# Kernel optimization log

Hardware: AMD Instinct MI355X
Metric: run time of the kernel (lower is better)

The kernel has to match this reference:

```python
import jax, jax.numpy as jnp
import numpy as np

N = 20000   # nodes
E = 320000  # edges
H = 4       # attention heads
GAT_SLOPE = 0.2   # DGL GATv2Conv internal leaky_relu slope
ACT_SLOPE = 0.01  # nn.LeakyReLU default slope


def gatv2_layer(h, src, dst, Wl, Wr, attn, b):
    """DGL GATv2Conv (share_weights=False, bias=True, eval mode).
    h: [N, Fin]; Wl/Wr: [Fin, H*D]; attn: [H, D]; b: [H*D]. Returns [N, H, D]."""
    n = h.shape[0]
    Hh, D = attn.shape
    fs = (h @ Wl).reshape(n, Hh, D)  # source projection
    fd = (h @ Wr).reshape(n, Hh, D)  # destination projection
    # edge-wise GATv2 score: a^T leaky_relu(Wl h_u + Wr h_v)
    e = jax.nn.leaky_relu(fs[src] + fd[dst], negative_slope=GAT_SLOPE)  # [E,H,D]
    logit = jnp.einsum('ehd,hd->eh', e, attn)  # [E,H]
    # edge softmax over incoming edges of each dst node (numerically stable)
    m = jax.ops.segment_max(logit, dst, num_segments=n)
    a = jnp.exp(logit - m[dst])
    s = jax.ops.segment_sum(a, dst, num_segments=n)
    alpha = a / s[dst]  # [E,H]
    out = jax.ops.segment_sum(alpha[:, :, None] * fs[src], dst, num_segments=n)
    return out + b.reshape(1, Hh, D)


def setup_inputs() -> dict:
    key = jax.random.key(0)
    ks = jax.random.split(key, 16)

    def w(k, shape, fan_in):
        return (jax.random.normal(k, shape, jnp.float32) / np.float32(np.sqrt(fan_in)))

    return {
        'n_feat': jax.random.normal(ks[0], (N, 512), jnp.float32),
        'src': jax.random.randint(ks[1], (E,), 0, N, jnp.int32),
        'dst': jax.random.randint(ks[2], (E,), 0, N, jnp.int32),
        # layer 0: 512 -> H x 128
        'Wl0': w(ks[3], (512, H * 128), 512), 'Wr0': w(ks[4], (512, H * 128), 512),
        'attn0': w(ks[5], (H, 128), 128), 'b0': jnp.zeros((H * 128,), jnp.float32),
        # layer 1: 128 -> H x 128
        'Wl1': w(ks[6], (128, H * 128), 128), 'Wr1': w(ks[7], (128, H * 128), 128),
        'attn1': w(ks[8], (H, 128), 128), 'b1': jnp.zeros((H * 128,), jnp.float32),
        # layer 2 (output): 128 -> H x 64
        'Wl2': w(ks[9], (128, H * 64), 128), 'Wr2': w(ks[10], (128, H * 64), 128),
        'attn2': w(ks[11], (H, 64), 64), 'b2': jnp.zeros((H * 64,), jnp.float32),
    }


def reference(n_feat, src, dst, Wl0, Wr0, attn0, b0, Wl1, Wr1, attn1, b1,
              Wl2, Wr2, attn2, b2):
    h = n_feat.reshape(n_feat.shape[0], -1)  # nn.Flatten
    for (Wl, Wr, attn, b) in ((Wl0, Wr0, attn0, b0),
                              (Wl1, Wr1, attn1, b1),
                              (Wl2, Wr2, attn2, b2)):
        h = gatv2_layer(h, src, dst, Wl, Wr, attn, b)  # [N,H,D]
        h = h.mean(axis=1)                              # head mean
        h = jax.nn.leaky_relu(h, negative_slope=ACT_SLOPE)
    # dgl.mean_nodes: per-graph mean readout (single graph -> [1, out])
    return h.mean(axis=0, keepdims=True)
```

## Files before the change

### kernel.cpp

```cpp
#include <hip/hip_runtime.h>
#include <hip/hip_bf16.h>
#include <stdint.h>


#define GAT_SLOPE 0.2f
#define ACT_SLOPE 0.01f
#define MAXDEG 64

typedef _Float16 half8 __attribute__((ext_vector_type(8)));
typedef _Float16 v2h __attribute__((ext_vector_type(2)));
typedef float floatx4 __attribute__((ext_vector_type(4)));

struct TransDesc {
  const float* src;
  _Float16* dst;
  int K, M, off;
};
struct PreArgs {
  TransDesc d[6];
  int wTotal;
  const float* nf;
  _Float16* A0;
  int aTotal;
  const int* src;
  const int* dst;
  int* counts;
  int* pcsrc;
  int E;
};

__global__ __launch_bounds__(256) void preproc_kernel(PreArgs pa) {
  int i = blockIdx.x * 256 + threadIdx.x;
  const int total = pa.wTotal + pa.aTotal + pa.E;
  if (i >= total) return;
  if (i < pa.wTotal) {
    int q = 0;
#pragma unroll
    for (int j = 1; j < 6; ++j)
      if (i >= pa.d[j].off) q = j;
    int local = i - pa.d[q].off;
    int K = pa.d[q].K, M = pa.d[q].M;
    int m = local / K, k = local % K;
    pa.d[q].dst[local] = (_Float16)pa.d[q].src[(size_t)k * M + m];
  } else if (i < pa.wTotal + pa.aTotal) {
    int j = i - pa.wTotal;
    pa.A0[j] = (_Float16)pa.nf[j];
  } else {
    int e = i - pa.wTotal - pa.aTotal;
    int d = pa.dst[e];
    int pos = atomicAdd(&pa.counts[d], 1);
    if (pos < MAXDEG) pa.pcsrc[(size_t)d * MAXDEG + pos] = pa.src[e];
  }
}

__device__ __forceinline__ void gload_lds16(const _Float16* g, _Float16* l) {
  __builtin_amdgcn_global_load_lds(
      (__attribute__((address_space(1))) unsigned int*)g,
      (__attribute__((address_space(3))) unsigned int*)l, 16, 0, 0);
}

#define TM 128
#define TN 128
#define TK 32

__global__ __launch_bounds__(256) void gemm_mfma_dual_kernel(
    const _Float16* __restrict__ A, const _Float16* __restrict__ B0,
    const _Float16* __restrict__ B1, _Float16* __restrict__ C0,
    _Float16* __restrict__ C1, int Nrow, int K, int M, int nStrips,
    int nbxLog2) {
  const int id = blockIdx.x;
  const int xcd = id & 7;
  const int s = id >> 3;
  const int nbx = 1 << nbxLog2;
  const int col = s & (nbx - 1);
  const int chunk = s >> nbxLog2;
  const int strip = chunk * 8 + xcd;
  if (strip >= nStrips) return;

  const int nb = nbx >> 1;
  const bool second = col >= nb;
  const _Float16* B = second ? B1 : B0;
  _Float16* C = second ? C1 : C0;
  const int bn = (second ? col - nb : col) * TN;
  const int bm = strip * TM;

  __shared__ __align__(16) _Float16 As[TM * TK];
  __shared__ __align__(16) _Float16 Bs[TN * TK];

  const int tid = threadIdx.x;
  const int w = tid >> 6;
  const int lane = tid & 63;
  const int wr = w >> 1;
  const int wc = w & 1;
  const int quad = lane >> 4;
  const int lr = lane & 15;

  const int lrow = lane >> 2;
  const int loff = (lane & 3) * 8;

  floatx4 acc[4][4];
#pragma unroll
  for (int i = 0; i < 4; ++i)
#pragma unroll
    for (int j = 0; j < 4; ++j) acc[i][j] = (floatx4){0.f, 0.f, 0.f, 0.f};

  const int KT = K / TK;
  for (int kt = 0; kt < KT; ++kt) {
    const int k0 = kt * TK;
#pragma unroll
    for (int half = 0; half < 2; ++half) {
      const int r0 = w * 32 + half * 16;
      int ga = bm + r0 + lrow;
      if (ga >= Nrow) ga = Nrow - 1;
      gload_lds16(A + (size_t)ga * K + k0 + loff, As + r0 * TK);
      gload_lds16(B + (size_t)(bn + r0 + lrow) * K + k0 + loff, Bs + r0 * TK);
    }
    __syncthreads();

    half8 ar[4], br[4];
#pragma unroll
    for (int i = 0; i < 4; ++i) {
      int row = wr * 64 + i * 16 + lr;
      ar[i] = *(const half8*)(As + row * TK + quad * 8);
    }
#pragma unroll
    for (int j = 0; j < 4; ++j) {
      int colr = wc * 64 + j * 16 + lr;
      br[j] = *(const half8*)(Bs + colr * TK + quad * 8);
    }
#pragma unroll
    for (int i = 0; i < 4; ++i)
#pragma unroll
      for (int j = 0; j < 4; ++j)
        acc[i][j] = __builtin_amdgcn_mfma_f32_16x16x32_f16(ar[i], br[j],
                                                           acc[i][j], 0, 0, 0);
    __syncthreads();
  }

#pragma unroll
  for (int i = 0; i < 4; ++i) {
#pragma unroll
    for (int r = 0; r < 4; ++r) {
      int row = bm + wr * 64 + i * 16 + quad * 4 + r;
      if (row >= Nrow) continue;
#pragma unroll
      for (int j = 0; j < 4; ++j) {
        int colc = bn + wc * 64 + j * 16 + lr;
        C[(size_t)row * M + colc] = (_Float16)acc[i][j][r];
      }
    }
  }
}

template <int D>
__global__ __launch_bounds__(128) void node_attn_kernel(
    const _Float16* __restrict__ fs, const _Float16* __restrict__ fd,
    const int* __restrict__ counts, const int* __restrict__ pcsrc,
    const float* __restrict__ attn, const float* __restrict__ bias,
    float* __restrict__ hout, _Float16* __restrict__ oh, int N) {
  constexpr int HD = 4 * D;
  constexpr int R = HD / 64;
  constexpr int R2 = R / 2;
  typedef _Float16 halfR __attribute__((ext_vector_type(R)));
  union Frag {
    halfR v;
    v2h h[R2];
    _Float16 s[R];
  };
  const int v = blockIdx.x;
  if (v >= N) return;
  const int wid = threadIdx.x >> 6;
  const int lane = threadIdx.x & 63;

  const v2h slope2 = {(_Float16)GAT_SLOPE, (_Float16)GAT_SLOPE};

  Frag fdv;
  fdv.v = *(const halfR*)(fd + (size_t)v * HD + lane * R);
  v2h ar2[R2];
#pragma unroll
  for (int j = 0; j < R2; ++j) {
    ar2[j][0] = (_Float16)attn[lane * R + 2 * j];
    ar2[j][1] = (_Float16)attn[lane * R + 2 * j + 1];
  }

  float m = -INFINITY, l = 0.f;
  float O[R];
#pragma unroll
  for (int i = 0; i < R; ++i) O[i] = 0.f;

  const int cnt = min(counts[v], MAXDEG);
  const int* elist = pcsrc + (size_t)v * MAXDEG;
  const int mid = (cnt + 1) >> 1;
  int k = wid ? mid : 0;
  const int ke = wid ? cnt : mid;

  for (; k + 3 < ke; k += 4) {
    const int s0 = elist[k];
    const int s1 = elist[k + 1];
    const int s2 = elist[k + 2];
    const int s3 = elist[k + 3];
    Frag t0, t1, t2, t3;
    t0.v = *(const halfR*)(fs + (size_t)s0 * HD + lane * R);
    t1.v = *(const halfR*)(fs + (size_t)s1 * HD + lane * R);
    t2.v = *(const halfR*)(fs + (size_t)s2 * HD + lane * R);
    t3.v = *(const halfR*)(fs + (size_t)s3 * HD + lane * R);
    float p0 = 0.f, p1 = 0.f, p2 = 0.f, p3 = 0.f;
#pragma unroll
    for (int j = 0; j < R2; ++j) {
      v2h x0 = t0.h[j] + fdv.h[j];
      v2h x1 = t1.h[j] + fdv.h[j];
      v2h x2 = t2.h[j] + fdv.h[j];
      v2h x3 = t3.h[j] + fdv.h[j];
      x0 = __builtin_elementwise_max(x0, x0 * slope2);
      x1 = __builtin_elementwise_max(x1, x1 * slope2);
      x2 = __builtin_elementwise_max(x2, x2 * slope2);
      x3 = __builtin_elementwise_max(x3, x3 * slope2);
      p0 = __builtin_amdgcn_fdot2(ar2[j], x0, p0, false);
      p1 = __builtin_amdgcn_fdot2(ar2[j], x1, p1, false);
      p2 = __builtin_amdgcn_fdot2(ar2[j], x2, p2, false);
      p3 = __builtin_amdgcn_fdot2(ar2[j], x3, p3, false);
    }
#pragma unroll
    for (int off = 1; off <= 8; off <<= 1) {
      p0 += __shfl_xor(p0, off, 64);
      p1 += __shfl_xor(p1, off, 64);
      p2 += __shfl_xor(p2, off, 64);
      p3 += __shfl_xor(p3, off, 64);
    }
    const float mq = fmaxf(fmaxf(p0, p1), fmaxf(p2, p3));
    const float w0 = __expf(p0 - mq);
    const float w1 = __expf(p1 - mq);
    const float w2 = __expf(p2 - mq);
    const float w3 = __expf(p3 - mq);
    const float mnew = fmaxf(m, mq);
    const float sc = __expf(m - mnew);
    const float sq = __expf(mq - mnew);
    l = l * sc + (w0 + w1 + w2 + w3) * sq;
#pragma unroll
    for (int i = 0; i < R; ++i) {
      float acc = (float)t0.s[i] * w0;
      acc = fmaf((float)t1.s[i], w1, acc);
      acc = fmaf((float)t2.s[i], w2, acc);
      acc = fmaf((float)t3.s[i], w3, acc);
      O[i] = fmaf(O[i], sc, sq * acc);
    }
    m = mnew;
  }
  for (; k < ke; ++k) {
    const int s0 = elist[k];
    Frag t0;
    t0.v = *(const halfR*)(fs + (size_t)s0 * HD + lane * R);
    float p0 = 0.f;
#pragma unroll
    for (int j = 0; j < R2; ++j) {
      v2h x0 = t0.h[j] + fdv.h[j];
      x0 = __builtin_elementwise_max(x0, x0 * slope2);
      p0 = __builtin_amdgcn_fdot2(ar2[j], x0, p0, false);
    }
#pragma unroll
    for (int off = 1; off <= 8; off <<= 1) p0 += __shfl_xor(p0, off, 64);
    const float mnew = fmaxf(m, p0);
    const float sc = __expf(m - mnew);
    const float p = __expf(p0 - mnew);
    l = l * sc + p;
#pragma unroll
    for (int i = 0; i < R; ++i) O[i] = fmaf(O[i], sc, p * (float)t0.s[i]);
    m = mnew;
  }

  __shared__ float sO[64 * R];
  __shared__ float sM[64];
  __shared__ float sL[64];
  if (wid == 1) {
    sM[lane] = m;
    sL[lane] = l;
#pragma unroll
    for (int i = 0; i < R; ++i) sO[lane * R + i] = O[i];
  }
  __syncthreads();
  if (wid == 1) return;
  {
    const float m1 = sM[lane];
    const float l1 = sL[lane];
    const float mstar = fmaxf(m, m1);
    const float a0 = (l > 0.f) ? __expf(m - mstar) : 0.f;
    const float a1 = (l1 > 0.f) ? __expf(m1 - mstar) : 0.f;
    l = l * a0 + l1 * a1;
#pragma unroll
    for (int i = 0; i < R; ++i) O[i] = O[i] * a0 + sO[lane * R + i] * a1;
  }

  const float inv = (l > 0.f) ? 1.f / l : 0.f;
#pragma unroll
  for (int i = 0; i < R; ++i) O[i] = O[i] * inv + bias[lane * R + i];
#pragma unroll
  for (int i = 0; i < R; ++i) {
    O[i] += __shfl_xor(O[i], 16, 64);
    O[i] += __shfl_xor(O[i], 32, 64);
    float x = O[i] * 0.25f;
    O[i] = x > 0.f ? x : x * ACT_SLOPE;
  }
  if (lane < 16) {
    const size_t base = (size_t)v * D + lane * R;
    if (hout) {
#pragma unroll
      for (int i = 0; i < R; ++i) hout[base + i] = O[i];
    }
    if (oh) {
#pragma unroll
      for (int i = 0; i < R; ++i) oh[base + i] = (_Float16)O[i];
    }
  }
}

__global__ __launch_bounds__(64) void final_mean_kernel(
    const float* __restrict__ h, float* __restrict__ out, int N) {
  const int d = threadIdx.x;
  float acc = 0.f;
  for (int n = blockIdx.x; n < N; n += gridDim.x) acc += h[(size_t)n * 64 + d];
  atomicAdd(&out[d], acc / (float)N);
}

extern "C" void kernel_launch(void* const* d_in, const int* in_sizes, int n_in,
                              void* d_out, int out_size, void* d_ws,
                              size_t ws_size, hipStream_t stream) {
  const float* n_feat = (const float*)d_in[0];
  const int* src = (const int*)d_in[1];
  const int* dst = (const int*)d_in[2];
  const float* Wl[3] = {(const float*)d_in[3], (const float*)d_in[7],
                        (const float*)d_in[11]};
  const float* Wr[3] = {(const float*)d_in[4], (const float*)d_in[8],
                        (const float*)d_in[12]};
  const float* attn[3] = {(const float*)d_in[5], (const float*)d_in[9],
                          (const float*)d_in[13]};
  const float* bias[3] = {(const float*)d_in[6], (const float*)d_in[10],
                          (const float*)d_in[14]};

  const int N = in_sizes[0] / 512;
  const int E = in_sizes[1];
  const int Kdim[3] = {512, 128, 128};
  const int Mdim[3] = {512, 512, 256};

  char* ws = (char*)d_ws;
  size_t o = 0;
  auto alloc = [&](size_t bytes) {
    void* p = ws + o;
    o += (bytes + 15) & ~(size_t)15;
    return p;
  };
  _Float16* fs = (_Float16*)alloc((size_t)N * 512 * 2);
  _Float16* fd = (_Float16*)alloc((size_t)N * 512 * 2);
  _Float16* A0 = (_Float16*)alloc((size_t)N * 512 * 2);
  _Float16* h1 = (_Float16*)alloc((size_t)N * 128 * 2);
  _Float16* h2 = (_Float16*)alloc((size_t)N * 128 * 2);
  float* hfin = (float*)alloc((size_t)N * 64 * 4);
  _Float16 *WlT[3], *WrT[3];
  for (int L = 0; L < 3; ++L) {
    size_t sz = (size_t)Kdim[L] * Mdim[L] * 2;
    WlT[L] = (_Float16*)alloc(sz);
    WrT[L] = (_Float16*)alloc(sz);
  }
  int* counts = (int*)alloc((size_t)N * 4);
  int* pcsrc = (int*)alloc((size_t)N * MAXDEG * 4);

  hipMemsetAsync(counts, 0, (size_t)N * sizeof(int), stream);
  {
    PreArgs pa;
    int off = 0;
    for (int L = 0; L < 3; ++L) {
      pa.d[2 * L] = {Wl[L], WlT[L], Kdim[L], Mdim[L], off};
      off += Kdim[L] * Mdim[L];
      pa.d[2 * L + 1] = {Wr[L], WrT[L], Kdim[L], Mdim[L], off};
      off += Kdim[L] * Mdim[L];
    }
    pa.wTotal = off;
    pa.nf = n_feat;
    pa.A0 = A0;
    pa.aTotal = N * 512;
    pa.src = src;
    pa.dst = dst;
    pa.counts = counts;
    pa.pcsrc = pcsrc;
    pa.E = E;
    int total = pa.wTotal + pa.aTotal + pa.E;
    preproc_kernel<<<(total + 255) / 256, 256, 0, stream>>>(pa);
  }

  const _Float16* Ain[3] = {A0, h1, h2};

  const int nStrips = (N + TM - 1) / TM;
  const int S8 = ((nStrips + 7) / 8) * 8;

  for (int L = 0; L < 3; ++L) {
    const int K = Kdim[L], M = Mdim[L];
    const int nbx = 2 * M / TN;
    const int nbxLog2 = (nbx == 8) ? 3 : 2;
    gemm_mfma_dual_kernel<<<S8 * nbx, 256, 0, stream>>>(
        Ain[L], WlT[L], WrT[L], fs, fd, N, K, M, nStrips, nbxLog2);
    if (L == 0) {
      node_attn_kernel<128><<<N, 128, 0, stream>>>(fs, fd, counts, pcsrc,
                                                   attn[L], bias[L], nullptr,
                                                   h1, N);
    } else if (L == 1) {
      node_attn_kernel<128><<<N, 128, 0, stream>>>(fs, fd, counts, pcsrc,
                                                   attn[L], bias[L], nullptr,
                                                   h2, N);
    } else {
      node_attn_kernel<64><<<N, 128, 0, stream>>>(fs, fd, counts, pcsrc,
                                                  attn[L], bias[L], hfin,
                                                  nullptr, N);
    }
  }

  hipMemsetAsync(d_out, 0, 64 * sizeof(float), stream);
  final_mean_kernel<<<256, 64, 0, stream>>>(hfin, (float*)d_out, N);
}
```

Measured before the change: 357.6 us.

## Use one wave per node in attention, fuse final mean, drop output memset

The node attention kernel now gives each 64-lane wave a whole node instead of splitting a node's edges across two waves and merging them through shared memory. Blocks hold four waves, so four nodes run per block. The last layer reduces its outputs into a shared-memory accumulator and atomically adds the mean straight into the output. This removes the hfin buffer, the final mean kernel and the output memset, whose zeroing moves into the preprocessing kernel. The cost is that per-node latency is no longer split across waves, and the last layer uses shared-memory atomics plus a grid-stride loop over 1024 blocks.

```diff
diff --git a/kernel.cpp b/kernel.cpp
--- a/kernel.cpp
+++ b/kernel.cpp
@@ -6,18 +6,18 @@
 #define GAT_SLOPE 0.2f
 #define ACT_SLOPE 0.01f
 #define MAXDEG 64
+#define TM 128
+#define TN 128
+#define TK 32
 
 typedef _Float16 half8 __attribute__((ext_vector_type(8)));
 typedef _Float16 v2h __attribute__((ext_vector_type(2)));
 typedef float floatx4 __attribute__((ext_vector_type(4)));
 
-struct TransDesc {
-  const float* src;
-  _Float16* dst;
-  int K, M, off;
-};
 struct PreArgs {
-  TransDesc d[6];
+  const float* W[6];
+  _Float16* WT[6];
+  int wK[6], wM[6], wOff[6];
   int wTotal;
   const float* nf;
   _Float16* A0;
@@ -27,26 +27,29 @@
   int* counts;
   int* pcsrc;
   int E;
+  float* dout;
 };
 
 __global__ __launch_bounds__(256) void preproc_kernel(PreArgs pa) {
   int i = blockIdx.x * 256 + threadIdx.x;
-  const int total = pa.wTotal + pa.aTotal + pa.E;
+  const int total = pa.wTotal + pa.aTotal + 64 + pa.E;
   if (i >= total) return;
   if (i < pa.wTotal) {
     int q = 0;
 #pragma unroll
     for (int j = 1; j < 6; ++j)
-      if (i >= pa.d[j].off) q = j;
-    int local = i - pa.d[q].off;
-    int K = pa.d[q].K, M = pa.d[q].M;
+      if (i >= pa.wOff[j]) q = j;
+    int local = i - pa.wOff[q];
+    int K = pa.wK[q], M = pa.wM[q];
     int m = local / K, k = local % K;
-    pa.d[q].dst[local] = (_Float16)pa.d[q].src[(size_t)k * M + m];
+    pa.WT[q][local] = (_Float16)pa.W[q][(size_t)k * M + m];
   } else if (i < pa.wTotal + pa.aTotal) {
     int j = i - pa.wTotal;
     pa.A0[j] = (_Float16)pa.nf[j];
+  } else if (i < pa.wTotal + pa.aTotal + 64) {
+    pa.dout[i - pa.wTotal - pa.aTotal] = 0.f;
   } else {
-    int e = i - pa.wTotal - pa.aTotal;
+    int e = i - pa.wTotal - pa.aTotal - 64;
     int d = pa.dst[e];
     int pos = atomicAdd(&pa.counts[d], 1);
     if (pos < MAXDEG) pa.pcsrc[(size_t)d * MAXDEG + pos] = pa.src[e];
@@ -58,10 +61,6 @@
       (__attribute__((address_space(1))) unsigned int*)g,
       (__attribute__((address_space(3))) unsigned int*)l, 16, 0, 0);
 }
-
-#define TM 128
-#define TN 128
-#define TK 32
 
 __global__ __launch_bounds__(256) void gemm_mfma_dual_kernel(
     const _Float16* __restrict__ A, const _Float16* __restrict__ B0,
@@ -94,7 +93,6 @@
   const int wc = w & 1;
   const int quad = lane >> 4;
   const int lr = lane & 15;
-
   const int lrow = lane >> 2;
   const int loff = (lane & 3) * 8;
 
@@ -152,12 +150,12 @@
   }
 }
 
-template <int D>
-__global__ __launch_bounds__(128) void node_attn_kernel(
+template <int D, bool LAST>
+__global__ __launch_bounds__(256) void node_attn_kernel(
     const _Float16* __restrict__ fs, const _Float16* __restrict__ fd,
     const int* __restrict__ counts, const int* __restrict__ pcsrc,
-    const float* __restrict__ attn, const float* __restrict__ bias,
-    float* __restrict__ hout, _Float16* __restrict__ oh, int N) {
+    const float* __restrict__ aw, const float* __restrict__ bias,
+    _Float16* __restrict__ oh, float* __restrict__ dout, int N) {
   constexpr int HD = 4 * D;
   constexpr int R = HD / 64;
   constexpr int R2 = R / 2;
@@ -167,158 +165,141 @@
     v2h h[R2];
     _Float16 s[R];
   };
-  const int v = blockIdx.x;
-  if (v >= N) return;
+  __shared__ float facc[64];
   const int wid = threadIdx.x >> 6;
   const int lane = threadIdx.x & 63;
-
   const v2h slope2 = {(_Float16)GAT_SLOPE, (_Float16)GAT_SLOPE};
 
-  Frag fdv;
-  fdv.v = *(const halfR*)(fd + (size_t)v * HD + lane * R);
+  if (LAST) {
+    if (threadIdx.x < 64) facc[threadIdx.x] = 0.f;
+    __syncthreads();
+  }
+
   v2h ar2[R2];
 #pragma unroll
   for (int j = 0; j < R2; ++j) {
-    ar2[j][0] = (_Float16)attn[lane * R + 2 * j];
-    ar2[j][1] = (_Float16)attn[lane * R + 2 * j + 1];
-  }
-
-  float m = -INFINITY, l = 0.f;
-  float O[R];
-#pragma unroll
-  for (int i = 0; i < R; ++i) O[i] = 0.f;
-
-  const int cnt = min(counts[v], MAXDEG);
-  const int* elist = pcsrc + (size_t)v * MAXDEG;
-  const int mid = (cnt + 1) >> 1;
-  int k = wid ? mid : 0;
-  const int ke = wid ? cnt : mid;
-
-  for (; k + 3 < ke; k += 4) {
-    const int s0 = elist[k];
-    const int s1 = elist[k + 1];
-    const int s2 = elist[k + 2];
-    const int s3 = elist[k + 3];
-    Frag t0, t1, t2, t3;
-    t0.v = *(const halfR*)(fs + (size_t)s0 * HD + lane * R);
-    t1.v = *(const halfR*)(fs + (size_t)s1 * HD + lane * R);
-    t2.v = *(const halfR*)(fs + (size_t)s2 * HD + lane * R);
-    t3.v = *(const halfR*)(fs + (size_t)s3 * HD + lane * R);
-    float p0 = 0.f, p1 = 0.f, p2 = 0.f, p3 = 0.f;
-#pragma unroll
-    for (int j = 0; j < R2; ++j) {
-      v2h x0 = t0.h[j] + fdv.h[j];
-      v2h x1 = t1.h[j] + fdv.h[j];
-      v2h x2 = t2.h[j] + fdv.h[j];
-      v2h x3 = t3.h[j] + fdv.h[j];
-      x0 = __builtin_elementwise_max(x0, x0 * slope2);
-      x1 = __builtin_elementwise_max(x1, x1 * slope2);
-      x2 = __builtin_elementwise_max(x2, x2 * slope2);
-      x3 = __builtin_elementwise_max(x3, x3 * slope2);
-      p0 = __builtin_amdgcn_fdot2(ar2[j], x0, p0, false);
-      p1 = __builtin_amdgcn_fdot2(ar2[j], x1, p1, false);
-      p2 = __builtin_amdgcn_fdot2(ar2[j], x2, p2, false);
-      p3 = __builtin_amdgcn_fdot2(ar2[j], x3, p3, false);
-    }
-#pragma unroll
-    for (int off = 1; off <= 8; off <<= 1) {
-      p0 += __shfl_xor(p0, off, 64);
-      p1 += __shfl_xor(p1, off, 64);
-      p2 += __shfl_xor(p2, off, 64);
-      p3 += __shfl_xor(p3, off, 64);
-    }
-    const float mq = fmaxf(fmaxf(p0, p1), fmaxf(p2, p3));
-    const float w0 = __expf(p0 - mq);
-    const float w1 = __expf(p1 - mq);
-    const float w2 = __expf(p2 - mq);
-    const float w3 = __expf(p3 - mq);
-    const float mnew = fmaxf(m, mq);
-    const float sc = __expf(m - mnew);
-    const float sq = __expf(mq - mnew);
-    l = l * sc + (w0 + w1 + w2 + w3) * sq;
-#pragma unroll
-    for (int i = 0; i < R; ++i) {
-      float acc = (float)t0.s[i] * w0;
-      acc = fmaf((float)t1.s[i], w1, acc);
-      acc = fmaf((float)t2.s[i], w2, acc);
-      acc = fmaf((float)t3.s[i], w3, acc);
-      O[i] = fmaf(O[i], sc, sq * acc);
-    }
-    m = mnew;
-  }
-  for (; k < ke; ++k) {
-    const int s0 = elist[k];
-    Frag t0;
-    t0.v = *(const halfR*)(fs + (size_t)s0 * HD + lane * R);
-    float p0 = 0.f;
-#pragma unroll
-    for (int j = 0; j < R2; ++j) {
-      v2h x0 = t0.h[j] + fdv.h[j];
-      x0 = __builtin_elementwise_max(x0, x0 * slope2);
-      p0 = __builtin_amdgcn_fdot2(ar2[j], x0, p0, false);
-    }
-#pragma unroll
-    for (int off = 1; off <= 8; off <<= 1) p0 += __shfl_xor(p0, off, 64);
-    const float mnew = fmaxf(m, p0);
-    const float sc = __expf(m - mnew);
-    const float p = __expf(p0 - mnew);
-    l = l * sc + p;
-#pragma unroll
-    for (int i = 0; i < R; ++i) O[i] = fmaf(O[i], sc, p * (float)t0.s[i]);
-    m = mnew;
-  }
-
-  __shared__ float sO[64 * R];
-  __shared__ float sM[64];
-  __shared__ float sL[64];
-  if (wid == 1) {
-    sM[lane] = m;
-    sL[lane] = l;
-#pragma unroll
-    for (int i = 0; i < R; ++i) sO[lane * R + i] = O[i];
-  }
-  __syncthreads();
-  if (wid == 1) return;
-  {
-    const float m1 = sM[lane];
-    const float l1 = sL[lane];
-    const float mstar = fmaxf(m, m1);
-    const float a0 = (l > 0.f) ? __expf(m - mstar) : 0.f;
-    const float a1 = (l1 > 0.f) ? __expf(m1 - mstar) : 0.f;
-    l = l * a0 + l1 * a1;
-#pragma unroll
-    for (int i = 0; i < R; ++i) O[i] = O[i] * a0 + sO[lane * R + i] * a1;
-  }
-
-  const float inv = (l > 0.f) ? 1.f / l : 0.f;
-#pragma unroll
-  for (int i = 0; i < R; ++i) O[i] = O[i] * inv + bias[lane * R + i];
-#pragma unroll
-  for (int i = 0; i < R; ++i) {
-    O[i] += __shfl_xor(O[i], 16, 64);
-    O[i] += __shfl_xor(O[i], 32, 64);
-    float x = O[i] * 0.25f;
-    O[i] = x > 0.f ? x : x * ACT_SLOPE;
-  }
-  if (lane < 16) {
-    const size_t base = (size_t)v * D + lane * R;
-    if (hout) {
-#pragma unroll
-      for (int i = 0; i < R; ++i) hout[base + i] = O[i];
-    }
-    if (oh) {
-#pragma unroll
-      for (int i = 0; i < R; ++i) oh[base + i] = (_Float16)O[i];
-    }
-  }
-}
-
-__global__ __launch_bounds__(64) void final_mean_kernel(
-    const float* __restrict__ h, float* __restrict__ out, int N) {
-  const int d = threadIdx.x;
-  float acc = 0.f;
-  for (int n = blockIdx.x; n < N; n += gridDim.x) acc += h[(size_t)n * 64 + d];
-  atomicAdd(&out[d], acc / (float)N);
+    ar2[j][0] = (_Float16)aw[lane * R + 2 * j];
+    ar2[j][1] = (_Float16)aw[lane * R + 2 * j + 1];
+  }
+  float br[R];
+#pragma unroll
+  for (int i = 0; i < R; ++i) br[i] = bias[lane * R + i];
+
+  for (int v0 = blockIdx.x * 4; v0 < N; v0 += gridDim.x * 4) {
+    const int v = v0 + wid;
+    if (v < N) {
+      Frag fdv;
+      fdv.v = *(const halfR*)(fd + (size_t)v * HD + lane * R);
+      float m = -INFINITY, l = 0.f;
+      float O[R];
+#pragma unroll
+      for (int i = 0; i < R; ++i) O[i] = 0.f;
+
+      const int cnt = min(counts[v], MAXDEG);
+      const int* elist = pcsrc + (size_t)v * MAXDEG;
+      int k = 0;
+      for (; k + 3 < cnt; k += 4) {
+        const int s0 = elist[k];
+        const int s1 = elist[k + 1];
+        const int s2 = elist[k + 2];
+        const int s3 = elist[k + 3];
+        Frag t0, t1, t2, t3;
+        t0.v = *(const halfR*)(fs + (size_t)s0 * HD + lane * R);
+        t1.v = *(const halfR*)(fs + (size_t)s1 * HD + lane * R);
+        t2.v = *(const halfR*)(fs + (size_t)s2 * HD + lane * R);
+        t3.v = *(const halfR*)(fs + (size_t)s3 * HD + lane * R);
+        float p0 = 0.f, p1 = 0.f, p2 = 0.f, p3 = 0.f;
+#pragma unroll
+        for (int j = 0; j < R2; ++j) {
+          v2h x0 = t0.h[j] + fdv.h[j];
+          v2h x1 = t1.h[j] + fdv.h[j];
+          v2h x2 = t2.h[j] + fdv.h[j];
+          v2h x3 = t3.h[j] + fdv.h[j];
+          x0 = __builtin_elementwise_max(x0, x0 * slope2);
+          x1 = __builtin_elementwise_max(x1, x1 * slope2);
+          x2 = __builtin_elementwise_max(x2, x2 * slope2);
+          x3 = __builtin_elementwise_max(x3, x3 * slope2);
+          p0 = __builtin_amdgcn_fdot2(ar2[j], x0, p0, false);
+          p1 = __builtin_amdgcn_fdot2(ar2[j], x1, p1, false);
+          p2 = __builtin_amdgcn_fdot2(ar2[j], x2, p2, false);
+          p3 = __builtin_amdgcn_fdot2(ar2[j], x3, p3, false);
+        }
+#pragma unroll
+        for (int off = 1; off <= 8; off <<= 1) {
+          p0 += __shfl_xor(p0, off, 64);
+          p1 += __shfl_xor(p1, off, 64);
+          p2 += __shfl_xor(p2, off, 64);
+          p3 += __shfl_xor(p3, off, 64);
+        }
+        const float mq = fmaxf(fmaxf(p0, p1), fmaxf(p2, p3));
+        const float w0 = __expf(p0 - mq);
+        const float w1 = __expf(p1 - mq);
+        const float w2 = __expf(p2 - mq);
+        const float w3 = __expf(p3 - mq);
+        const float mnew = fmaxf(m, mq);
+        const float sc = __expf(m - mnew);
+        const float sq = __expf(mq - mnew);
+        l = l * sc + (w0 + w1 + w2 + w3) * sq;
+#pragma unroll
+        for (int i = 0; i < R; ++i) {
+          float acc = (float)t0.s[i] * w0;
+          acc = fmaf((float)t1.s[i], w1, acc);
+          acc = fmaf((float)t2.s[i], w2, acc);
+          acc = fmaf((float)t3.s[i], w3, acc);
+          O[i] = fmaf(O[i], sc, sq * acc);
+        }
+        m = mnew;
+      }
+      for (; k < cnt; ++k) {
+        const int s0 = elist[k];
+        Frag t0;
+        t0.v = *(const halfR*)(fs + (size_t)s0 * HD + lane * R);
+        float p0 = 0.f;
+#pragma unroll
+        for (int j = 0; j < R2; ++j) {
+          v2h x0 = t0.h[j] + fdv.h[j];
+          x0 = __builtin_elementwise_max(x0, x0 * slope2);
+          p0 = __builtin_amdgcn_fdot2(ar2[j], x0, p0, false);
+        }
+#pragma unroll
+        for (int off = 1; off <= 8; off <<= 1) p0 += __shfl_xor(p0, off, 64);
+        const float mnew = fmaxf(m, p0);
+        const float sc = __expf(m - mnew);
+        const float p = __expf(p0 - mnew);
+        l = l * sc + p;
+#pragma unroll
+        for (int i = 0; i < R; ++i) O[i] = fmaf(O[i], sc, p * (float)t0.s[i]);
+        m = mnew;
+      }
+
+      const float inv = (l > 0.f) ? 1.f / l : 0.f;
+#pragma unroll
+      for (int i = 0; i < R; ++i) O[i] = O[i] * inv + br[i];
+#pragma unroll
+      for (int i = 0; i < R; ++i) {
+        O[i] += __shfl_xor(O[i], 16, 64);
+        O[i] += __shfl_xor(O[i], 32, 64);
+        float x = O[i] * 0.25f;
+        O[i] = x > 0.f ? x : x * ACT_SLOPE;
+      }
+      if (lane < 16) {
+        if (!LAST) {
+          const size_t base = (size_t)v * D + lane * R;
+#pragma unroll
+          for (int i = 0; i < R; ++i) oh[base + i] = (_Float16)O[i];
+        } else {
+#pragma unroll
+          for (int i = 0; i < R; ++i) atomicAdd(&facc[lane * R + i], O[i]);
+        }
+      }
+    }
+  }
+
+  if (LAST) {
+    __syncthreads();
+    if (threadIdx.x < 64)
+      atomicAdd(&dout[threadIdx.x], facc[threadIdx.x] / (float)N);
+  }
 }
 
 extern "C" void kernel_launch(void* const* d_in, const int* in_sizes, int n_in,
@@ -331,8 +312,8 @@
                         (const float*)d_in[11]};
   const float* Wr[3] = {(const float*)d_in[4], (const float*)d_in[8],
                         (const float*)d_in[12]};
-  const float* attn[3] = {(const float*)d_in[5], (const float*)d_in[9],
-                          (const float*)d_in[13]};
+  const float* attnw[3] = {(const float*)d_in[5], (const float*)d_in[9],
+                           (const float*)d_in[13]};
   const float* bias[3] = {(const float*)d_in[6], (const float*)d_in[10],
                           (const float*)d_in[14]};
 
@@ -353,24 +334,30 @@
   _Float16* A0 = (_Float16*)alloc((size_t)N * 512 * 2);
   _Float16* h1 = (_Float16*)alloc((size_t)N * 128 * 2);
   _Float16* h2 = (_Float16*)alloc((size_t)N * 128 * 2);
-  float* hfin = (float*)alloc((size_t)N * 64 * 4);
-  _Float16 *WlT[3], *WrT[3];
+  _Float16* WT[6];
   for (int L = 0; L < 3; ++L) {
     size_t sz = (size_t)Kdim[L] * Mdim[L] * 2;
-    WlT[L] = (_Float16*)alloc(sz);
-    WrT[L] = (_Float16*)alloc(sz);
+    WT[2 * L] = (_Float16*)alloc(sz);
+    WT[2 * L + 1] = (_Float16*)alloc(sz);
   }
   int* counts = (int*)alloc((size_t)N * 4);
   int* pcsrc = (int*)alloc((size_t)N * MAXDEG * 4);
 
   hipMemsetAsync(counts, 0, (size_t)N * sizeof(int), stream);
+
   {
     PreArgs pa;
     int off = 0;
     for (int L = 0; L < 3; ++L) {
-      pa.d[2 * L] = {Wl[L], WlT[L], Kdim[L], Mdim[L], off};
+      pa.W[2 * L] = Wl[L];
+      pa.W[2 * L + 1] = Wr[L];
+      pa.WT[2 * L] = WT[2 * L];
+      pa.WT[2 * L + 1] = WT[2 * L + 1];
+      pa.wK[2 * L] = pa.wK[2 * L + 1] = Kdim[L];
+      pa.wM[2 * L] = pa.wM[2 * L + 1] = Mdim[L];
+      pa.wOff[2 * L] = off;
       off += Kdim[L] * Mdim[L];
-      pa.d[2 * L + 1] = {Wr[L], WrT[L], Kdim[L], Mdim[L], off};
+      pa.wOff[2 * L + 1] = off;
       off += Kdim[L] * Mdim[L];
     }
     pa.wTotal = off;
@@ -382,11 +369,14 @@
     pa.counts = counts;
     pa.pcsrc = pcsrc;
     pa.E = E;
-    int total = pa.wTotal + pa.aTotal + pa.E;
+    pa.dout = (float*)d_out;
+    int total = pa.wTotal + pa.aTotal + 64 + E;
     preproc_kernel<<<(total + 255) / 256, 256, 0, stream>>>(pa);
   }
 
   const _Float16* Ain[3] = {A0, h1, h2};
+  _Float16* WlT[3] = {WT[0], WT[2], WT[4]};
+  _Float16* WrT[3] = {WT[1], WT[3], WT[5]};
 
   const int nStrips = (N + TM - 1) / TM;
   const int S8 = ((nStrips + 7) / 8) * 8;
@@ -398,20 +388,14 @@
     gemm_mfma_dual_kernel<<<S8 * nbx, 256, 0, stream>>>(
         Ain[L], WlT[L], WrT[L], fs, fd, N, K, M, nStrips, nbxLog2);
     if (L == 0) {
-      node_attn_kernel<128><<<N, 128, 0, stream>>>(fs, fd, counts, pcsrc,
-                                                   attn[L], bias[L], nullptr,
-                                                   h1, N);
+      node_attn_kernel<128, false><<<(N + 3) / 4, 256, 0, stream>>>(
+          fs, fd, counts, pcsrc, attnw[0], bias[0], h1, nullptr, N);
     } else if (L == 1) {
-      node_attn_kernel<128><<<N, 128, 0, stream>>>(fs, fd, counts, pcsrc,
-                                                   attn[L], bias[L], nullptr,
-                                                   h2, N);
+      node_attn_kernel<128, false><<<(N + 3) / 4, 256, 0, stream>>>(
+          fs, fd, counts, pcsrc, attnw[1], bias[1], h2, nullptr, N);
     } else {
-      node_attn_kernel<64><<<N, 128, 0, stream>>>(fs, fd, counts, pcsrc,
-                                                  attn[L], bias[L], hfin,
-                                                  nullptr, N);
-    }
-  }
-
-  hipMemsetAsync(d_out, 0, 64 * sizeof(float), stream);
-  final_mean_kernel<<<256, 64, 0, stream>>>(hfin, (float*)d_out, N);
+      node_attn_kernel<64, true><<<1024, 256, 0, stream>>>(
+          fs, fd, counts, pcsrc, attnw[2], bias[2], nullptr, (float*)d_out, N);
+    }
+  }
 }
```

New measurement: 359.4 us. No clear change (+0.5%).
